# Optimization experiments

Hardware: AMD Instinct MI355X
Metric: run time of the kernel (lower is better)

## Reference

```python
import jax, jax.numpy as jnp
import numpy as np

B, S, D, H = 256, 128, 2, 512


def _lstm_cell(x, h, c, Wih, Whh, bih, bhh):
    # PyTorch LSTMCell gate order: i, f, g, o
    z = x @ Wih.T + bih + h @ Whh.T + bhh
    i, f, g, o = jnp.split(z, 4, axis=-1)
    c_new = jax.nn.sigmoid(f) * c + jax.nn.sigmoid(i) * jnp.tanh(g)
    h_new = jax.nn.sigmoid(o) * jnp.tanh(c_new)
    return h_new, c_new


def setup_inputs() -> dict:
    key = jax.random.key(0)
    ks = jax.random.split(key, 16)
    sc = 0.05
    inp = {
        "x": jax.random.uniform(ks[0], (B, S, D), dtype=jnp.float32),
        "enc_Wih": jax.random.normal(ks[1], (4 * H, D), dtype=jnp.float32) * sc,
        "enc_Whh": jax.random.normal(ks[2], (4 * H, H), dtype=jnp.float32) * sc,
        "enc_bih": jax.random.normal(ks[3], (4 * H,), dtype=jnp.float32) * sc,
        "enc_bhh": jax.random.normal(ks[4], (4 * H,), dtype=jnp.float32) * sc,
        "dec_Wih": jax.random.normal(ks[5], (4 * H, H), dtype=jnp.float32) * sc,
        "dec_Whh": jax.random.normal(ks[6], (4 * H, H), dtype=jnp.float32) * sc,
        "dec_bih": jax.random.normal(ks[7], (4 * H,), dtype=jnp.float32) * sc,
        "dec_bhh": jax.random.normal(ks[8], (4 * H,), dtype=jnp.float32) * sc,
        "W1": jax.random.normal(ks[9], (H, H), dtype=jnp.float32) * sc,
        "b1": jax.random.normal(ks[10], (H,), dtype=jnp.float32) * sc,
        "W2": jax.random.normal(ks[11], (H, H), dtype=jnp.float32) * sc,
        "b2": jax.random.normal(ks[12], (H,), dtype=jnp.float32) * sc,
        "v": jax.random.normal(ks[13], (1, H), dtype=jnp.float32) * sc,
        "bv": jax.random.normal(ks[14], (1,), dtype=jnp.float32) * sc,
    }
    return inp


def reference(x, enc_Wih, enc_Whh, enc_bih, enc_bhh,
              dec_Wih, dec_Whh, dec_bih, dec_bhh,
              W1, b1, W2, b2, v, bv):
    # ---- encoder: LSTMCell scan over sequence ----
    def enc_step(carry, xt):
        h, c = carry
        h, c = _lstm_cell(xt, h, c, enc_Wih, enc_Whh, enc_bih, enc_bhh)
        return (h, c), h

    h0 = jnp.zeros((B, H), dtype=x.dtype)
    c0 = jnp.zeros((B, H), dtype=x.dtype)
    (h_enc, c_enc), enc_hs = jax.lax.scan(enc_step, (h0, c0),
                                          jnp.transpose(x, (1, 0, 2)))
    enc_hs = jnp.transpose(enc_hs, (1, 0, 2))          # [B, S, H]
    W1e = enc_hs @ W1.T + b1                            # [B, S, H]

    # ---- decoder with per-step additive attention ----
    dec_in = jnp.full((B, H), -1.0, dtype=x.dtype)      # constant decoder input

    def dec_step(carry, _):
        h, c = carry
        h, c = _lstm_cell(dec_in, h, c, dec_Wih, dec_Whh, dec_bih, dec_bhh)
        W2h = h @ W2.T + b2                             # [B, H]
        u = jnp.tanh(W1e + W2h[:, None, :]) @ v[0] + bv[0]  # [B, S]
        a = jax.nn.softmax(u, axis=1)                   # [B, S]
        h_new = jnp.einsum('bs,bsh->bh', a, enc_hs)     # attention glimpse
        return (h_new, c), a

    _, attn = jax.lax.scan(dec_step, (h_enc, c_enc), None, length=S)
    return jnp.transpose(attn, (1, 0, 2))               # [B, S, S]
```

## Files before the change

### kernel.cpp

```cpp
#include <hip/hip_runtime.h>

#define B_ 256
#define S_ 128
#define D_ 2
#define H_ 512
#define W2TP 528

__device__ __forceinline__ float sigm(float x){ return 1.f/(1.f+__expf(-x)); }
__device__ __forceinline__ float tanh_(float x){ return 1.f - 2.f/(__expf(2.f*x)+1.f); }

__global__ __launch_bounds__(256) void prep4(
    const float* __restrict__ dWih, const float* __restrict__ dbih,
    const float* __restrict__ dbhh, const float* __restrict__ ebih,
    const float* __restrict__ ebhh, const float* __restrict__ W2,
    float* __restrict__ dxw, float* __restrict__ ebias, float* __restrict__ W2Tp)
{
    int bx = blockIdx.x, tid = threadIdx.x;
    if (bx < 8) {
        int j = bx * 256 + tid;
        const float* row = dWih + (size_t)j * H_;
        float s = 0.f;
        for (int k = 0; k < H_; k++) s += row[k];
        dxw[j]   = dbih[j] + dbhh[j] - s;
        ebias[j] = ebih[j] + ebhh[j];
    } else {
        int i = (bx - 8) * 256 + tid;
        int k = i >> 9, j = i & 511;
        W2Tp[(size_t)k * W2TP + j] = W2[(size_t)j * H_ + k];
    }
}

__global__ __launch_bounds__(256) void pack_whh(
    const float* __restrict__ eW, const float* __restrict__ dW,
    float* __restrict__ pe, float* __restrict__ pd)
{
    size_t n = (size_t)blockIdx.x * 256 + threadIdx.x;
    int sel = (int)(n >> 20);
    int m = (int)(n & 1048575);
    int c = m & 3, rw = (m >> 2) & 63, i4 = (m >> 8) & 15;
    int ks = (m >> 12) & 7, jt = m >> 15;
    int g = rw >> 4, hu = rw & 15;
    size_t src = (size_t)(g * H_ + jt * 16 + hu) * H_ + ks * 64 + i4 * 4 + c;
    if (sel) pd[m] = dW[src]; else pe[m] = eW[src];
}

template<bool ENC>
__global__ __launch_bounds__(512) void lstm_step4(
    const float* __restrict__ Wsrc, int packed,
    const float* __restrict__ h_in, long hstr, int hzero,
    float* __restrict__ c_st, int czero,
    const float* __restrict__ xbias,
    const float* __restrict__ Wih, const float* __restrict__ xt,
    float* __restrict__ h_out, long hostr)
{
    __shared__ float smem[8704];
    float (*Hs)[H_]     = (float (*)[H_])smem;
    float (*P)[16][68]  = (float (*)[16][68])smem;

    const int tid = threadIdx.x;
    const int rw = tid & 63;
    const int ks = tid >> 6;
    const int bx = blockIdx.x;
    const int bt = bx & 15, jt = bx >> 4;
    const int b0 = bt * 16;
    const int g = rw >> 4, hu = rw & 15;

    float w[64];
    if (packed) {
        const float4* wp = (const float4*)Wsrc + (size_t)(jt * 8 + ks) * 1024 + rw;
#pragma unroll
        for (int i = 0; i < 16; i++) {
            float4 t4 = wp[(size_t)i * 64];
            w[4*i+0]=t4.x; w[4*i+1]=t4.y; w[4*i+2]=t4.z; w[4*i+3]=t4.w;
        }
    } else {
        const float4* wp = (const float4*)(Wsrc + (size_t)(g * H_ + jt * 16 + hu) * H_ + ks * 64);
#pragma unroll
        for (int i = 0; i < 16; i++) {
            float4 t4 = wp[i];
            w[4*i+0]=t4.x; w[4*i+1]=t4.y; w[4*i+2]=t4.z; w[4*i+3]=t4.w;
        }
    }

    float acc[16];
#pragma unroll
    for (int b = 0; b < 16; b++) acc[b] = 0.f;

    if (!hzero) {
        {
            int r = tid >> 5, c0 = (tid & 31) * 4;
            const float* hr = h_in + (size_t)(b0 + r) * hstr;
#pragma unroll
            for (int i = 0; i < 4; i++)
                *(float4*)&Hs[r][c0 + i * 128] = *(const float4*)(hr + c0 + i * 128);
        }
        __syncthreads();
#pragma unroll 2
        for (int b = 0; b < 16; b++) {
            const float4* hp = (const float4*)&Hs[b][ks * 64];
            float s = 0.f;
#pragma unroll
            for (int i = 0; i < 16; i++) {
                float4 h4 = hp[i];
                s += h4.x*w[4*i] + h4.y*w[4*i+1] + h4.z*w[4*i+2] + h4.w*w[4*i+3];
            }
            acc[b] = s;
        }
        __syncthreads();
    }

#pragma unroll
    for (int b = 0; b < 16; b++) P[ks][b][rw] = acc[b];
    __syncthreads();

    if (tid < 256) {
        int b = tid & 15, h2 = tid >> 4;
        float z[4];
#pragma unroll
        for (int gg = 0; gg < 4; gg++) {
            int row = gg * 16 + h2;
            float s = 0.f;
#pragma unroll
            for (int k8 = 0; k8 < 8; k8++) s += P[k8][b][row];
            z[gg] = s + xbias[gg * H_ + jt * 16 + h2];
        }
        int bb = b0 + b, hj = jt * 16 + h2;
        if constexpr (ENC) {
            float x0 = xt[(size_t)bb * (S_ * D_) + 0];
            float x1 = xt[(size_t)bb * (S_ * D_) + 1];
#pragma unroll
            for (int gg = 0; gg < 4; gg++)
                z[gg] += x0 * Wih[(size_t)(gg * H_ + hj) * D_ + 0]
                       + x1 * Wih[(size_t)(gg * H_ + hj) * D_ + 1];
        }
        float cold = czero ? 0.f : c_st[(size_t)bb * H_ + hj];
        float cn = sigm(z[1]) * cold + sigm(z[0]) * tanh_(z[2]);
        float hn = sigm(z[3]) * tanh_(cn);
        c_st[(size_t)bb * H_ + hj] = cn;
        h_out[(size_t)bb * hostr + hj] = hn;
    }
}

__global__ __launch_bounds__(512) void w2h_step(
    const float* __restrict__ W2Tp, const float* __restrict__ b2,
    const float* __restrict__ h_dec, float* __restrict__ w2h)
{
    __shared__ float smem[8704];
    float (*Hs)[H_]    = (float (*)[H_])smem;
    float (*P2)[16][17] = (float (*)[16][17])smem;

    const int tid = threadIdx.x;
    const int ks = tid >> 6, rw = tid & 63;
    const int ksub = rw >> 4, j = rw & 15;
    const int bx = blockIdx.x;
    const int bt = bx & 15, jt = bx >> 4;
    const int b0 = bt * 16, j0 = jt * 16;

    {
        int r = tid >> 5, c0 = (tid & 31) * 4;
        const float* hr = h_dec + (size_t)(b0 + r) * H_;
#pragma unroll
        for (int i = 0; i < 4; i++)
            *(float4*)&Hs[r][c0 + i * 128] = *(const float4*)(hr + c0 + i * 128);
    }
    __syncthreads();

    const int kk = ks * 64 + ksub * 16;
    float w2r[16];
#pragma unroll
    for (int i = 0; i < 16; i++) w2r[i] = W2Tp[(size_t)(kk + i) * W2TP + j0 + j];

    float acc[16];
#pragma unroll
    for (int b = 0; b < 16; b++) {
        float s = 0.f;
#pragma unroll
        for (int i = 0; i < 16; i++) s += Hs[b][kk + i] * w2r[i];
        acc[b] = s;
    }
    __syncthreads();
#pragma unroll
    for (int b = 0; b < 16; b++) P2[ks * 4 + ksub][b][j] = acc[b];
    __syncthreads();

    if (tid < 256) {
        int b = tid & 15, jj = tid >> 4;
        float s = 0.f;
#pragma unroll
        for (int p = 0; p < 32; p++) s += P2[p][b][jj];
        w2h[(size_t)(b0 + b) * H_ + j0 + jj] = s + b2[j0 + jj];
    }
}

template<int BM, int BN, int TM, int TN>
__global__ __launch_bounds__((BM/TM)*(BN/TN)) void gemm_bias(
    const float* __restrict__ A, const float* __restrict__ Bm,
    const float* __restrict__ bias, float* __restrict__ C,
    int M, int N, int K)
{
    constexpr int BK = 32;
    constexpr int TH = (BM / TM) * (BN / TN);
    constexpr int AL = BM * BK / TH;
    constexpr int BL = BN * BK / TH;
    constexpr int RP = TH / BK;
    __shared__ float As[BK][BM + 4];
    __shared__ float Bs[BK][BN + 4];
    const int tid = threadIdx.x;
    const int tn = tid % (BN / TN);
    const int tm = tid / (BN / TN);
    const int m0 = blockIdx.x * BM, n0 = blockIdx.y * BN;
    const int lk = tid % BK, lr = tid / BK;

    float acc[TM][TN];
#pragma unroll
    for (int i = 0; i < TM; i++)
#pragma unroll
        for (int j = 0; j < TN; j++) acc[i][j] = 0.f;

    float areg[AL], breg[BL];
#pragma unroll
    for (int i = 0; i < AL; i++) areg[i] = A[(size_t)(m0 + lr + i * RP) * K + lk];
#pragma unroll
    for (int i = 0; i < BL; i++) breg[i] = Bm[(size_t)(n0 + lr + i * RP) * K + lk];

    const int NC = K / BK;
    for (int c = 0; c < NC; c++) {
        __syncthreads();
#pragma unroll
        for (int i = 0; i < AL; i++) As[lk][lr + i * RP] = areg[i];
#pragma unroll
        for (int i = 0; i < BL; i++) Bs[lk][lr + i * RP] = breg[i];
        __syncthreads();
        if (c + 1 < NC) {
            int k0 = (c + 1) * BK;
#pragma unroll
            for (int i = 0; i < AL; i++) areg[i] = A[(size_t)(m0 + lr + i * RP) * K + k0 + lk];
#pragma unroll
            for (int i = 0; i < BL; i++) breg[i] = Bm[(size_t)(n0 + lr + i * RP) * K + k0 + lk];
        }
#pragma unroll
        for (int k = 0; k < BK; k++) {
            float av[TM], bvv[TN];
#pragma unroll
            for (int i = 0; i < TM; i++) av[i] = As[k][tm * TM + i];
#pragma unroll
            for (int j = 0; j < TN; j++) bvv[j] = Bs[k][tn * TN + j];
#pragma unroll
            for (int i = 0; i < TM; i++)
#pragma unroll
                for (int j = 0; j < TN; j++) acc[i][j] += av[i] * bvv[j];
        }
    }
#pragma unroll
    for (int i = 0; i < TM; i++) {
        int m = m0 + tm * TM + i;
#pragma unroll
        for (int j = 0; j < TN; j++) {
            int n = n0 + tn * TN + j;
            C[(size_t)m * N + n] = acc[i][j] + bias[n];
        }
    }
}

__global__ __launch_bounds__(512) void attn_step(
    const float* __restrict__ w2h, const float* __restrict__ vv,
    const float* __restrict__ bv, const float* __restrict__ W1e,
    const float* __restrict__ enc_hs, float* __restrict__ out,
    float* __restrict__ h_glim, int t)
{
    __shared__ float ua[S_];
    __shared__ float red[8];
    const int tid = threadIdx.x;
    const int b = blockIdx.x;
    const int ln = tid & 63, wv = tid >> 6;

    float4 q0 = *(const float4*)(w2h + (size_t)b * H_ + ln * 8);
    float4 q1 = *(const float4*)(w2h + (size_t)b * H_ + ln * 8 + 4);
    float4 v0 = *(const float4*)(vv + ln * 8);
    float4 v1 = *(const float4*)(vv + ln * 8 + 4);
    const float bvr = bv[0];
    const float* w1b = W1e + (size_t)b * S_ * H_;
#pragma unroll 2
    for (int si = 0; si < 16; si++) {
        int s = wv * 16 + si;
        const float4* rp = (const float4*)(w1b + (size_t)s * H_ + ln * 8);
        float4 r0 = rp[0], r1 = rp[1];
        float sum = tanh_(r0.x + q0.x) * v0.x + tanh_(r0.y + q0.y) * v0.y
                  + tanh_(r0.z + q0.z) * v0.z + tanh_(r0.w + q0.w) * v0.w
                  + tanh_(r1.x + q1.x) * v1.x + tanh_(r1.y + q1.y) * v1.y
                  + tanh_(r1.z + q1.z) * v1.z + tanh_(r1.w + q1.w) * v1.w;
#pragma unroll
        for (int off = 32; off; off >>= 1) sum += __shfl_xor(sum, off);
        if (ln == 0) ua[s] = sum + bvr;
    }
    __syncthreads();

    float e = 0.f;
    if (tid < 128) {
        float m = ua[tid];
#pragma unroll
        for (int off = 32; off; off >>= 1) m = fmaxf(m, __shfl_xor(m, off));
        if (ln == 0) red[tid >> 6] = m;
    }
    __syncthreads();
    if (tid < 128) {
        float mx = fmaxf(red[0], red[1]);
        e = __expf(ua[tid] - mx);
        float ss = e;
#pragma unroll
        for (int off = 32; off; off >>= 1) ss += __shfl_xor(ss, off);
        if (ln == 0) red[2 + (tid >> 6)] = ss;
    }
    __syncthreads();
    if (tid < 128) {
        float a = e / (red[2] + red[3]);
        ua[tid] = a;
        out[(size_t)b * S_ * S_ + (size_t)t * S_ + tid] = a;
    }
    __syncthreads();

    const float* eb = enc_hs + (size_t)b * S_ * H_;
    float ga = 0.f;
#pragma unroll 4
    for (int s = 0; s < S_; s++) ga += ua[s] * eb[(size_t)s * H_ + tid];
    h_glim[(size_t)b * H_ + tid] = ga;
}

extern "C" void kernel_launch(void* const* d_in, const int* in_sizes, int n_in,
                              void* d_out, int out_size, void* d_ws, size_t ws_size,
                              hipStream_t stream)
{
    const float* x    = (const float*)d_in[0];
    const float* eWih = (const float*)d_in[1];
    const float* eWhh = (const float*)d_in[2];
    const float* ebih = (const float*)d_in[3];
    const float* ebhh = (const float*)d_in[4];
    const float* dWih = (const float*)d_in[5];
    const float* dWhh = (const float*)d_in[6];
    const float* dbih = (const float*)d_in[7];
    const float* dbhh = (const float*)d_in[8];
    const float* W1   = (const float*)d_in[9];
    const float* b1   = (const float*)d_in[10];
    const float* W2   = (const float*)d_in[11];
    const float* b2   = (const float*)d_in[12];
    const float* vv   = (const float*)d_in[13];
    const float* bv   = (const float*)d_in[14];
    float* out = (float*)d_out;

    float* ws     = (float*)d_ws;
    float* enc_hs = ws;
    float* W1e    = enc_hs + (size_t)B_ * S_ * H_;
    float* h_dec  = W1e    + (size_t)B_ * S_ * H_;
    float* h_glim = h_dec  + (size_t)B_ * H_;
    float* c_cur  = h_glim + (size_t)B_ * H_;
    float* w2h    = c_cur  + (size_t)B_ * H_;
    float* W2Tp   = w2h    + (size_t)B_ * H_;
    float* dxw    = W2Tp   + (size_t)H_ * W2TP;
    float* ebias  = dxw    + 2048;
    float* wpk_e  = ebias  + 2048;
    float* wpk_d  = wpk_e  + 1048576;

    size_t base_f = (size_t)(wpk_e - ws);
    int packed = (ws_size >= (base_f + 2097152u) * sizeof(float)) ? 1 : 0;

    prep4<<<1032, 256, 0, stream>>>(dWih, dbih, dbhh, ebih, ebhh, W2,
                                    dxw, ebias, W2Tp);
    if (packed)
        pack_whh<<<8192, 256, 0, stream>>>(eWhh, dWhh, wpk_e, wpk_d);

    const float* We = packed ? wpk_e : eWhh;
    const float* Wd = packed ? wpk_d : dWhh;

    for (int t = 0; t < S_; t++) {
        lstm_step4<true><<<512, 512, 0, stream>>>(
            We, packed,
            enc_hs + (size_t)(t - 1) * H_, (long)(S_ * H_), (t == 0) ? 1 : 0,
            c_cur, (t == 0) ? 1 : 0,
            ebias, eWih, x + (size_t)t * D_,
            enc_hs + (size_t)t * H_, (long)(S_ * H_));
    }

    gemm_bias<128, 128, 8, 8><<<dim3((B_ * S_) / 128, H_ / 128), 256, 0, stream>>>(
        enc_hs, W1, b1, W1e, B_ * S_, H_, H_);

    for (int t = 0; t < S_; t++) {
        const float* h_in = (t == 0) ? (enc_hs + (size_t)(S_ - 1) * H_) : h_glim;
        long hstr = (t == 0) ? (long)(S_ * H_) : (long)H_;
        lstm_step4<false><<<512, 512, 0, stream>>>(
            Wd, packed, h_in, hstr, 0,
            c_cur, 0, dxw, nullptr, nullptr,
            h_dec, (long)H_);
        w2h_step<<<512, 512, 0, stream>>>(W2Tp, b2, h_dec, w2h);
        attn_step<<<B_, 512, 0, stream>>>(w2h, vv, bv, W1e, enc_hs, out, h_glim, t);
    }
}
```

Baseline: 12.55 ms.

## Fuse per-step LSTM and attention launches into persistent kernels with grid barriers

Replaces the 128 encoder launches and the 384 decoder launches (LSTM, W2h, attention) with two persistent kernels of 256 blocks each. Steps are separated by a software grid barrier built on atomics. Weights, the cell state and the biases stay in registers across timesteps, and W2 is read directly instead of through a transposed copy. This removes per-launch overhead and weight reloads, but relies on all 256 blocks being co-resident and adds global-barrier latency, with cross-block data exchanged through agent-scope atomic loads and stores.

```diff
diff --git a/kernel.cpp b/kernel.cpp
--- a/kernel.cpp
+++ b/kernel.cpp
@@ -4,30 +4,48 @@
 #define S_ 128
 #define D_ 2
 #define H_ 512
-#define W2TP 528
+#define NBLK 256
 
 __device__ __forceinline__ float sigm(float x){ return 1.f/(1.f+__expf(-x)); }
 __device__ __forceinline__ float tanh_(float x){ return 1.f - 2.f/(__expf(2.f*x)+1.f); }
 
-__global__ __launch_bounds__(256) void prep4(
+__device__ __forceinline__ float ldc(const float* p){
+    return __hip_atomic_load(p, __ATOMIC_RELAXED, __HIP_MEMORY_SCOPE_AGENT);
+}
+__device__ __forceinline__ void stc(float* p, float v){
+    __hip_atomic_store(p, v, __ATOMIC_RELAXED, __HIP_MEMORY_SCOPE_AGENT);
+}
+
+__device__ __forceinline__ void gbar(unsigned* bar){
+    __syncthreads();
+    if (threadIdx.x == 0) {
+        asm volatile("s_waitcnt vmcnt(0)" ::: "memory");
+        unsigned g = __hip_atomic_load(&bar[1], __ATOMIC_RELAXED, __HIP_MEMORY_SCOPE_AGENT);
+        unsigned a = __hip_atomic_fetch_add(&bar[0], 1u, __ATOMIC_RELAXED, __HIP_MEMORY_SCOPE_AGENT);
+        if (a == NBLK - 1u) {
+            __hip_atomic_store(&bar[0], 0u, __ATOMIC_RELAXED, __HIP_MEMORY_SCOPE_AGENT);
+            asm volatile("s_waitcnt vmcnt(0)" ::: "memory");
+            __hip_atomic_store(&bar[1], g + 1u, __ATOMIC_RELAXED, __HIP_MEMORY_SCOPE_AGENT);
+        } else {
+            while (__hip_atomic_load(&bar[1], __ATOMIC_RELAXED, __HIP_MEMORY_SCOPE_AGENT) == g)
+                __builtin_amdgcn_s_sleep(1);
+        }
+    }
+    __syncthreads();
+}
+
+__global__ __launch_bounds__(256) void prep5(
     const float* __restrict__ dWih, const float* __restrict__ dbih,
     const float* __restrict__ dbhh, const float* __restrict__ ebih,
-    const float* __restrict__ ebhh, const float* __restrict__ W2,
-    float* __restrict__ dxw, float* __restrict__ ebias, float* __restrict__ W2Tp)
-{
-    int bx = blockIdx.x, tid = threadIdx.x;
-    if (bx < 8) {
-        int j = bx * 256 + tid;
-        const float* row = dWih + (size_t)j * H_;
-        float s = 0.f;
-        for (int k = 0; k < H_; k++) s += row[k];
-        dxw[j]   = dbih[j] + dbhh[j] - s;
-        ebias[j] = ebih[j] + ebhh[j];
-    } else {
-        int i = (bx - 8) * 256 + tid;
-        int k = i >> 9, j = i & 511;
-        W2Tp[(size_t)k * W2TP + j] = W2[(size_t)j * H_ + k];
-    }
+    const float* __restrict__ ebhh, float* __restrict__ dxw,
+    float* __restrict__ ebias)
+{
+    int j = blockIdx.x * 256 + threadIdx.x;
+    const float* row = dWih + (size_t)j * H_;
+    float s = 0.f;
+    for (int k = 0; k < H_; k++) s += row[k];
+    dxw[j]   = dbih[j] + dbhh[j] - s;
+    ebias[j] = ebih[j] + ebhh[j];
 }
 
 __global__ __launch_bounds__(256) void pack_whh(
@@ -44,152 +62,106 @@
     if (sel) pd[m] = dW[src]; else pe[m] = eW[src];
 }
 
-template<bool ENC>
-__global__ __launch_bounds__(512) void lstm_step4(
-    const float* __restrict__ Wsrc, int packed,
-    const float* __restrict__ h_in, long hstr, int hzero,
-    float* __restrict__ c_st, int czero,
-    const float* __restrict__ xbias,
-    const float* __restrict__ Wih, const float* __restrict__ xt,
-    float* __restrict__ h_out, long hostr)
-{
-    __shared__ float smem[8704];
-    float (*Hs)[H_]     = (float (*)[H_])smem;
-    float (*P)[16][68]  = (float (*)[16][68])smem;
-
-    const int tid = threadIdx.x;
-    const int rw = tid & 63;
-    const int ks = tid >> 6;
-    const int bx = blockIdx.x;
-    const int bt = bx & 15, jt = bx >> 4;
-    const int b0 = bt * 16;
-    const int g = rw >> 4, hu = rw & 15;
-
-    float w[64];
+__device__ __forceinline__ void load_w64(const float* Wsrc, int packed,
+                                         int jt, int ks, int rw, float* w)
+{
     if (packed) {
         const float4* wp = (const float4*)Wsrc + (size_t)(jt * 8 + ks) * 1024 + rw;
 #pragma unroll
         for (int i = 0; i < 16; i++) {
             float4 t4 = wp[(size_t)i * 64];
-            w[4*i+0]=t4.x; w[4*i+1]=t4.y; w[4*i+2]=t4.z; w[4*i+3]=t4.w;
+            w[4*i]=t4.x; w[4*i+1]=t4.y; w[4*i+2]=t4.z; w[4*i+3]=t4.w;
         }
     } else {
-        const float4* wp = (const float4*)(Wsrc + (size_t)(g * H_ + jt * 16 + hu) * H_ + ks * 64);
+        int g = rw >> 4, hu = rw & 15;
+        const float4* wp = (const float4*)(Wsrc + (size_t)(g * H_ + jt*16 + hu) * H_ + ks * 64);
 #pragma unroll
         for (int i = 0; i < 16; i++) {
             float4 t4 = wp[i];
-            w[4*i+0]=t4.x; w[4*i+1]=t4.y; w[4*i+2]=t4.z; w[4*i+3]=t4.w;
-        }
-    }
-
-    float acc[16];
-#pragma unroll
-    for (int b = 0; b < 16; b++) acc[b] = 0.f;
-
-    if (!hzero) {
-        {
-            int r = tid >> 5, c0 = (tid & 31) * 4;
-            const float* hr = h_in + (size_t)(b0 + r) * hstr;
-#pragma unroll
-            for (int i = 0; i < 4; i++)
-                *(float4*)&Hs[r][c0 + i * 128] = *(const float4*)(hr + c0 + i * 128);
-        }
-        __syncthreads();
-#pragma unroll 2
-        for (int b = 0; b < 16; b++) {
-            const float4* hp = (const float4*)&Hs[b][ks * 64];
-            float s = 0.f;
-#pragma unroll
-            for (int i = 0; i < 16; i++) {
-                float4 h4 = hp[i];
-                s += h4.x*w[4*i] + h4.y*w[4*i+1] + h4.z*w[4*i+2] + h4.w*w[4*i+3];
-            }
-            acc[b] = s;
-        }
-        __syncthreads();
-    }
-
-#pragma unroll
-    for (int b = 0; b < 16; b++) P[ks][b][rw] = acc[b];
-    __syncthreads();
-
-    if (tid < 256) {
-        int b = tid & 15, h2 = tid >> 4;
-        float z[4];
-#pragma unroll
-        for (int gg = 0; gg < 4; gg++) {
-            int row = gg * 16 + h2;
-            float s = 0.f;
-#pragma unroll
-            for (int k8 = 0; k8 < 8; k8++) s += P[k8][b][row];
-            z[gg] = s + xbias[gg * H_ + jt * 16 + h2];
-        }
-        int bb = b0 + b, hj = jt * 16 + h2;
-        if constexpr (ENC) {
-            float x0 = xt[(size_t)bb * (S_ * D_) + 0];
-            float x1 = xt[(size_t)bb * (S_ * D_) + 1];
-#pragma unroll
-            for (int gg = 0; gg < 4; gg++)
-                z[gg] += x0 * Wih[(size_t)(gg * H_ + hj) * D_ + 0]
-                       + x1 * Wih[(size_t)(gg * H_ + hj) * D_ + 1];
-        }
-        float cold = czero ? 0.f : c_st[(size_t)bb * H_ + hj];
-        float cn = sigm(z[1]) * cold + sigm(z[0]) * tanh_(z[2]);
-        float hn = sigm(z[3]) * tanh_(cn);
-        c_st[(size_t)bb * H_ + hj] = cn;
-        h_out[(size_t)bb * hostr + hj] = hn;
-    }
-}
-
-__global__ __launch_bounds__(512) void w2h_step(
-    const float* __restrict__ W2Tp, const float* __restrict__ b2,
-    const float* __restrict__ h_dec, float* __restrict__ w2h)
-{
-    __shared__ float smem[8704];
+            w[4*i]=t4.x; w[4*i+1]=t4.y; w[4*i+2]=t4.z; w[4*i+3]=t4.w;
+        }
+    }
+}
+
+__global__ __launch_bounds__(512, 1) void enc_p(
+    const float* __restrict__ x, const float* __restrict__ eWih,
+    const float* __restrict__ Wsrc, int packed,
+    const float* __restrict__ ebias, float* __restrict__ enc_hs,
+    float* __restrict__ c_fin, unsigned* bar)
+{
+    __shared__ float smem[16384];
     float (*Hs)[H_]    = (float (*)[H_])smem;
-    float (*P2)[16][17] = (float (*)[16][17])smem;
+    float (*P)[32][64] = (float (*)[32][64])smem;
 
     const int tid = threadIdx.x;
     const int ks = tid >> 6, rw = tid & 63;
-    const int ksub = rw >> 4, j = rw & 15;
-    const int bx = blockIdx.x;
-    const int bt = bx & 15, jt = bx >> 4;
-    const int b0 = bt * 16, j0 = jt * 16;
-
-    {
-        int r = tid >> 5, c0 = (tid & 31) * 4;
-        const float* hr = h_dec + (size_t)(b0 + r) * H_;
-#pragma unroll
-        for (int i = 0; i < 4; i++)
-            *(float4*)&Hs[r][c0 + i * 128] = *(const float4*)(hr + c0 + i * 128);
-    }
-    __syncthreads();
-
-    const int kk = ks * 64 + ksub * 16;
-    float w2r[16];
-#pragma unroll
-    for (int i = 0; i < 16; i++) w2r[i] = W2Tp[(size_t)(kk + i) * W2TP + j0 + j];
-
-    float acc[16];
-#pragma unroll
-    for (int b = 0; b < 16; b++) {
-        float s = 0.f;
-#pragma unroll
-        for (int i = 0; i < 16; i++) s += Hs[b][kk + i] * w2r[i];
-        acc[b] = s;
-    }
-    __syncthreads();
-#pragma unroll
-    for (int b = 0; b < 16; b++) P2[ks * 4 + ksub][b][j] = acc[b];
-    __syncthreads();
-
-    if (tid < 256) {
-        int b = tid & 15, jj = tid >> 4;
-        float s = 0.f;
-#pragma unroll
-        for (int p = 0; p < 32; p++) s += P2[p][b][jj];
-        w2h[(size_t)(b0 + b) * H_ + j0 + jj] = s + b2[j0 + jj];
-    }
+    const int bt = blockIdx.x >> 5, jt = blockIdx.x & 31;
+    const int b0 = bt * 32, hu0 = jt * 16;
+
+    float w[64];
+    load_w64(Wsrc, packed, jt, ks, rw, w);
+
+    const int fb = tid >> 4, fh = tid & 15;
+    const int fhu = hu0 + fh;
+    float eb4[4], wi0[4], wi1[4];
+#pragma unroll
+    for (int g = 0; g < 4; g++) {
+        eb4[g] = ebias[g*H_ + fhu];
+        wi0[g] = eWih[(size_t)(g*H_ + fhu)*D_ + 0];
+        wi1[g] = eWih[(size_t)(g*H_ + fhu)*D_ + 1];
+    }
+    float creg = 0.f;
+
+    for (int t = 0; t < S_; t++) {
+        float acc[32];
+        if (t == 0) {
+#pragma unroll
+            for (int b = 0; b < 32; b++) acc[b] = 0.f;
+        } else {
+#pragma unroll 4
+            for (int i = 0; i < 32; i++)
+                Hs[i][tid] = ldc(&enc_hs[((size_t)(b0+i)*S_ + (t-1))*H_ + tid]);
+            __syncthreads();
+#pragma unroll 2
+            for (int b = 0; b < 32; b++) {
+                const float4* hp = (const float4*)&Hs[b][ks * 64];
+                float s = 0.f;
+#pragma unroll
+                for (int i = 0; i < 16; i++) {
+                    float4 h4 = hp[i];
+                    s += h4.x*w[4*i] + h4.y*w[4*i+1] + h4.z*w[4*i+2] + h4.w*w[4*i+3];
+                }
+                acc[b] = s;
+            }
+            __syncthreads();
+        }
+#pragma unroll
+        for (int b = 0; b < 32; b++) P[ks][b][rw ^ ((b & 3) << 4)] = acc[b];
+        __syncthreads();
+        {
+            float z[4];
+#pragma unroll
+            for (int g = 0; g < 4; g++) {
+                int row = g*16 + fh;
+                float s2 = 0.f;
+#pragma unroll
+                for (int k8 = 0; k8 < 8; k8++)
+                    s2 += P[k8][fb][row ^ ((fb & 3) << 4)];
+                z[g] = s2 + eb4[g];
+            }
+            int bb = b0 + fb;
+            float x0 = x[((size_t)bb*S_ + t)*D_ + 0];
+            float x1 = x[((size_t)bb*S_ + t)*D_ + 1];
+#pragma unroll
+            for (int g = 0; g < 4; g++) z[g] += x0*wi0[g] + x1*wi1[g];
+            float cn = sigm(z[1])*creg + sigm(z[0])*tanh_(z[2]);
+            float hn = sigm(z[3])*tanh_(cn);
+            creg = cn;
+            stc(&enc_hs[((size_t)bb*S_ + t)*H_ + fhu], hn);
+        }
+        if (t < S_ - 1) gbar(bar);
+    }
+    stc(&c_fin[(size_t)(b0 + fb)*H_ + fhu], creg);
 }
 
 template<int BM, int BN, int TM, int TN>
@@ -262,68 +234,176 @@
     }
 }
 
-__global__ __launch_bounds__(512) void attn_step(
-    const float* __restrict__ w2h, const float* __restrict__ vv,
-    const float* __restrict__ bv, const float* __restrict__ W1e,
-    const float* __restrict__ enc_hs, float* __restrict__ out,
-    float* __restrict__ h_glim, int t)
-{
-    __shared__ float ua[S_];
-    __shared__ float red[8];
+__global__ __launch_bounds__(512, 1) void dec_p(
+    const float* __restrict__ Wsrc, int packed,
+    const float* __restrict__ dxw,
+    const float* __restrict__ W2, const float* __restrict__ b2,
+    const float* __restrict__ vv, const float* __restrict__ bv,
+    const float* __restrict__ enc_hs, const float* __restrict__ W1e,
+    const float* __restrict__ c_fin,
+    float* __restrict__ h_dec, float* __restrict__ w2h,
+    float* __restrict__ h_glim, float* __restrict__ out,
+    unsigned* bar)
+{
+    __shared__ float smem[16384];
+    float (*Hs)[H_]     = (float (*)[H_])smem;
+    float (*P)[32][64]  = (float (*)[32][64])smem;
+    float (*P2)[32][16] = (float (*)[32][16])smem;
+    float* qq  = smem;
+    float* ua  = smem + 512;
+    float* red = smem + 640;
+
     const int tid = threadIdx.x;
-    const int b = blockIdx.x;
+    const int ks = tid >> 6, rw = tid & 63;
+    const int bt = blockIdx.x >> 5, jt = blockIdx.x & 31;
+    const int b0 = bt * 32, hu0 = jt * 16;
     const int ln = tid & 63, wv = tid >> 6;
 
-    float4 q0 = *(const float4*)(w2h + (size_t)b * H_ + ln * 8);
-    float4 q1 = *(const float4*)(w2h + (size_t)b * H_ + ln * 8 + 4);
-    float4 v0 = *(const float4*)(vv + ln * 8);
-    float4 v1 = *(const float4*)(vv + ln * 8 + 4);
+    float w[64];
+    load_w64(Wsrc, packed, jt, ks, rw, w);
+
+    const int rsub = (tid >> 4) & 3, jj = tid & 15;
+    float w2r[16];
+    {
+        const float4* p4 = (const float4*)(W2 + (size_t)(hu0 + jj)*H_ + ks*64 + rsub*16);
+#pragma unroll
+        for (int i = 0; i < 4; i++) {
+            float4 t4 = p4[i];
+            w2r[4*i]=t4.x; w2r[4*i+1]=t4.y; w2r[4*i+2]=t4.z; w2r[4*i+3]=t4.w;
+        }
+    }
+
+    const int fb = tid >> 4, fh = tid & 15;
+    const int fhu = hu0 + fh;
+    float db4[4];
+#pragma unroll
+    for (int g = 0; g < 4; g++) db4[g] = dxw[g*H_ + fhu];
+    const float b2f = b2[fhu];
+    float creg = c_fin[(size_t)(b0 + fb)*H_ + fhu];
+
+    const int ab = blockIdx.x;
+    const float* w1b = W1e    + (size_t)ab * S_ * H_;
+    const float* eb  = enc_hs + (size_t)ab * S_ * H_;
+    const float4 vr0 = *(const float4*)(vv + ln*8);
+    const float4 vr1 = *(const float4*)(vv + ln*8 + 4);
     const float bvr = bv[0];
-    const float* w1b = W1e + (size_t)b * S_ * H_;
+
+    for (int t = 0; t < S_; t++) {
+        {
+            const float* hsrc = (t == 0) ? (enc_hs + (size_t)(S_-1)*H_) : h_glim;
+            const size_t hstr = (t == 0) ? (size_t)(S_*H_) : (size_t)H_;
+#pragma unroll 4
+            for (int i = 0; i < 32; i++)
+                Hs[i][tid] = ldc(&hsrc[(size_t)(b0+i)*hstr + tid]);
+            __syncthreads();
+            float acc[32];
 #pragma unroll 2
-    for (int si = 0; si < 16; si++) {
-        int s = wv * 16 + si;
-        const float4* rp = (const float4*)(w1b + (size_t)s * H_ + ln * 8);
-        float4 r0 = rp[0], r1 = rp[1];
-        float sum = tanh_(r0.x + q0.x) * v0.x + tanh_(r0.y + q0.y) * v0.y
-                  + tanh_(r0.z + q0.z) * v0.z + tanh_(r0.w + q0.w) * v0.w
-                  + tanh_(r1.x + q1.x) * v1.x + tanh_(r1.y + q1.y) * v1.y
-                  + tanh_(r1.z + q1.z) * v1.z + tanh_(r1.w + q1.w) * v1.w;
-#pragma unroll
-        for (int off = 32; off; off >>= 1) sum += __shfl_xor(sum, off);
-        if (ln == 0) ua[s] = sum + bvr;
-    }
-    __syncthreads();
-
-    float e = 0.f;
-    if (tid < 128) {
-        float m = ua[tid];
-#pragma unroll
-        for (int off = 32; off; off >>= 1) m = fmaxf(m, __shfl_xor(m, off));
-        if (ln == 0) red[tid >> 6] = m;
-    }
-    __syncthreads();
-    if (tid < 128) {
-        float mx = fmaxf(red[0], red[1]);
-        e = __expf(ua[tid] - mx);
-        float ss = e;
-#pragma unroll
-        for (int off = 32; off; off >>= 1) ss += __shfl_xor(ss, off);
-        if (ln == 0) red[2 + (tid >> 6)] = ss;
-    }
-    __syncthreads();
-    if (tid < 128) {
-        float a = e / (red[2] + red[3]);
-        ua[tid] = a;
-        out[(size_t)b * S_ * S_ + (size_t)t * S_ + tid] = a;
-    }
-    __syncthreads();
-
-    const float* eb = enc_hs + (size_t)b * S_ * H_;
-    float ga = 0.f;
+            for (int b = 0; b < 32; b++) {
+                const float4* hp = (const float4*)&Hs[b][ks * 64];
+                float s = 0.f;
+#pragma unroll
+                for (int i = 0; i < 16; i++) {
+                    float4 h4 = hp[i];
+                    s += h4.x*w[4*i] + h4.y*w[4*i+1] + h4.z*w[4*i+2] + h4.w*w[4*i+3];
+                }
+                acc[b] = s;
+            }
+            __syncthreads();
+#pragma unroll
+            for (int b = 0; b < 32; b++) P[ks][b][rw ^ ((b & 3) << 4)] = acc[b];
+            __syncthreads();
+            float z[4];
+#pragma unroll
+            for (int g = 0; g < 4; g++) {
+                int row = g*16 + fh;
+                float s2 = 0.f;
+#pragma unroll
+                for (int k8 = 0; k8 < 8; k8++)
+                    s2 += P[k8][fb][row ^ ((fb & 3) << 4)];
+                z[g] = s2 + db4[g];
+            }
+            float cn = sigm(z[1])*creg + sigm(z[0])*tanh_(z[2]);
+            float hn = sigm(z[3])*tanh_(cn);
+            creg = cn;
+            stc(&h_dec[(size_t)(b0 + fb)*H_ + fhu], hn);
+        }
+        gbar(bar);
+        {
 #pragma unroll 4
-    for (int s = 0; s < S_; s++) ga += ua[s] * eb[(size_t)s * H_ + tid];
-    h_glim[(size_t)b * H_ + tid] = ga;
+            for (int i = 0; i < 32; i++)
+                Hs[i][tid] = ldc(&h_dec[(size_t)(b0+i)*H_ + tid]);
+            __syncthreads();
+            float a2[32];
+#pragma unroll 2
+            for (int b = 0; b < 32; b++) {
+                const float4* hp = (const float4*)&Hs[b][ks*64 + rsub*16];
+                float s = 0.f;
+#pragma unroll
+                for (int i = 0; i < 4; i++) {
+                    float4 h4 = hp[i];
+                    s += h4.x*w2r[4*i] + h4.y*w2r[4*i+1] + h4.z*w2r[4*i+2] + h4.w*w2r[4*i+3];
+                }
+                a2[b] = s;
+            }
+            __syncthreads();
+#pragma unroll
+            for (int b = 0; b < 32; b++) P2[b][ks*4 + rsub][jj] = a2[b];
+            __syncthreads();
+            float s2 = 0.f;
+#pragma unroll
+            for (int p = 0; p < 32; p++) s2 += P2[fb][p][fh];
+            stc(&w2h[(size_t)(b0 + fb)*H_ + fhu], s2 + b2f);
+        }
+        gbar(bar);
+        {
+            qq[tid] = ldc(&w2h[(size_t)ab*H_ + tid]);
+            __syncthreads();
+            float4 q0 = *(float4*)&qq[ln*8];
+            float4 q1 = *(float4*)&qq[ln*8 + 4];
+#pragma unroll 2
+            for (int si = 0; si < 16; si++) {
+                int s = wv*16 + si;
+                const float4* rp = (const float4*)(w1b + (size_t)s*H_ + ln*8);
+                float4 r0 = rp[0], r1 = rp[1];
+                float sum = tanh_(r0.x+q0.x)*vr0.x + tanh_(r0.y+q0.y)*vr0.y
+                          + tanh_(r0.z+q0.z)*vr0.z + tanh_(r0.w+q0.w)*vr0.w
+                          + tanh_(r1.x+q1.x)*vr1.x + tanh_(r1.y+q1.y)*vr1.y
+                          + tanh_(r1.z+q1.z)*vr1.z + tanh_(r1.w+q1.w)*vr1.w;
+#pragma unroll
+                for (int off = 32; off; off >>= 1) sum += __shfl_xor(sum, off);
+                if (ln == 0) ua[s] = sum + bvr;
+            }
+            __syncthreads();
+            float e = 0.f;
+            if (tid < 128) {
+                float m = ua[tid];
+#pragma unroll
+                for (int off = 32; off; off >>= 1) m = fmaxf(m, __shfl_xor(m, off));
+                if (ln == 0) red[tid >> 6] = m;
+            }
+            __syncthreads();
+            if (tid < 128) {
+                float mx = fmaxf(red[0], red[1]);
+                e = __expf(ua[tid] - mx);
+                float ss = e;
+#pragma unroll
+                for (int off = 32; off; off >>= 1) ss += __shfl_xor(ss, off);
+                if (ln == 0) red[2 + (tid >> 6)] = ss;
+            }
+            __syncthreads();
+            if (tid < 128) {
+                float a = e / (red[2] + red[3]);
+                ua[tid] = a;
+                out[(size_t)ab*S_*S_ + (size_t)t*S_ + tid] = a;
+            }
+            __syncthreads();
+            float ga = 0.f;
+#pragma unroll 4
+            for (int s = 0; s < S_; s++) ga += ua[s] * eb[(size_t)s*H_ + tid];
+            stc(&h_glim[(size_t)ab*H_ + tid], ga);
+        }
+        if (t < S_ - 1) gbar(bar);
+    }
 }
 
 extern "C" void kernel_launch(void* const* d_in, const int* in_sizes, int n_in,
@@ -352,45 +432,31 @@
     float* W1e    = enc_hs + (size_t)B_ * S_ * H_;
     float* h_dec  = W1e    + (size_t)B_ * S_ * H_;
     float* h_glim = h_dec  + (size_t)B_ * H_;
-    float* c_cur  = h_glim + (size_t)B_ * H_;
-    float* w2h    = c_cur  + (size_t)B_ * H_;
-    float* W2Tp   = w2h    + (size_t)B_ * H_;
-    float* dxw    = W2Tp   + (size_t)H_ * W2TP;
+    float* w2h    = h_glim + (size_t)B_ * H_;
+    float* c_fin  = w2h    + (size_t)B_ * H_;
+    float* dxw    = c_fin  + (size_t)B_ * H_;
     float* ebias  = dxw    + 2048;
-    float* wpk_e  = ebias  + 2048;
-    float* wpk_d  = wpk_e  + 1048576;
+    unsigned* bars = (unsigned*)(ebias + 2048);
+    float* wpk_e  = (float*)(bars + 8);
+    float* wpk_d  = wpk_e + 1048576;
 
     size_t base_f = (size_t)(wpk_e - ws);
     int packed = (ws_size >= (base_f + 2097152u) * sizeof(float)) ? 1 : 0;
 
-    prep4<<<1032, 256, 0, stream>>>(dWih, dbih, dbhh, ebih, ebhh, W2,
-                                    dxw, ebias, W2Tp);
+    hipMemsetAsync(bars, 0, 8 * sizeof(unsigned), stream);
+    prep5<<<8, 256, 0, stream>>>(dWih, dbih, dbhh, ebih, ebhh, dxw, ebias);
     if (packed)
         pack_whh<<<8192, 256, 0, stream>>>(eWhh, dWhh, wpk_e, wpk_d);
 
     const float* We = packed ? wpk_e : eWhh;
     const float* Wd = packed ? wpk_d : dWhh;
 
-    for (int t = 0; t < S_; t++) {
-        lstm_step4<true><<<512, 512, 0, stream>>>(
-            We, packed,
-            enc_hs + (size_t)(t - 1) * H_, (long)(S_ * H_), (t == 0) ? 1 : 0,
-            c_cur, (t == 0) ? 1 : 0,
-            ebias, eWih, x + (size_t)t * D_,
-            enc_hs + (size_t)t * H_, (long)(S_ * H_));
-    }
+    enc_p<<<NBLK, 512, 0, stream>>>(x, eWih, We, packed, ebias, enc_hs, c_fin, bars);
 
     gemm_bias<128, 128, 8, 8><<<dim3((B_ * S_) / 128, H_ / 128), 256, 0, stream>>>(
         enc_hs, W1, b1, W1e, B_ * S_, H_, H_);
 
-    for (int t = 0; t < S_; t++) {
-        const float* h_in = (t == 0) ? (enc_hs + (size_t)(S_ - 1) * H_) : h_glim;
-        long hstr = (t == 0) ? (long)(S_ * H_) : (long)H_;
-        lstm_step4<false><<<512, 512, 0, stream>>>(
-            Wd, packed, h_in, hstr, 0,
-            c_cur, 0, dxw, nullptr, nullptr,
-            h_dec, (long)H_);
-        w2h_step<<<512, 512, 0, stream>>>(W2Tp, b2, h_dec, w2h);
-        attn_step<<<B_, 512, 0, stream>>>(w2h, vv, bv, W1e, enc_hs, out, h_glim, t);
-    }
-}
+    dec_p<<<NBLK, 512, 0, stream>>>(Wd, packed, dxw, W2, b2, vv, bv,
+                                    enc_hs, W1e, c_fin,
+                                    h_dec, w2h, h_glim, out, bars + 4);
+}
```

Result: slower. 16.14 ms (+28.6%).
